# Kernel optimization log

Measured on AMD Instinct MI355X. Metric: run time of the kernel, lower is better.

The kernel has to match this reference:

```python
import jax, jax.numpy as jnp
import numpy as np

B, N, F_IN, D, K, INTER = 64, 512, 128, 128, 32, 256
EPS = 1e-5


def _bn(x, g, b, axes):
    # BatchNorm in training mode (biased batch statistics), matching torch BN forward
    m = x.mean(axis=axes, keepdims=True)
    v = x.var(axis=axes, keepdims=True)
    return (x - m) * jax.lax.rsqrt(v + EPS) * g + b


def setup_inputs() -> dict:
    key = jax.random.key(0)
    ks = jax.random.split(key, 12)
    u = lambda k, s: jax.random.uniform(k, s, jnp.float32, -0.3, 0.3)
    return {
        "data": jax.random.normal(ks[0], (B, N, F_IN), jnp.float32),
        "emb_weight": u(ks[1], (N, D)),          # nn.Embedding(node_num, dim), kaiming-uniform-ish
        "lin_W": u(ks[2], (F_IN, D)),            # GraphLayer lin (no bias)
        "att_i": u(ks[3], (D,)),
        "att_j": u(ks[4], (D,)),
        "att_em_i": u(ks[5], (D,)),
        "att_em_j": u(ks[6], (D,)),
        "gnn_bias": jnp.zeros((D,), jnp.float32),
        "gnn_bn_g": jnp.ones((D,), jnp.float32),
        "gnn_bn_b": jnp.zeros((D,), jnp.float32),
        "bn_out_g": jnp.ones((D,), jnp.float32),
        "bn_out_b": jnp.zeros((D,), jnp.float32),
        "W1": u(ks[7], (D, INTER)), "b1": jnp.zeros((INTER,), jnp.float32),
        "bn1_g": jnp.ones((INTER,), jnp.float32), "bn1_b": jnp.zeros((INTER,), jnp.float32),
        "W2": u(ks[8], (INTER, INTER)), "b2": jnp.zeros((INTER,), jnp.float32),
        "bn2_g": jnp.ones((INTER,), jnp.float32), "bn2_b": jnp.zeros((INTER,), jnp.float32),
        "W3": u(ks[9], (INTER, 1)), "b3": jnp.zeros((1,), jnp.float32),
    }


def reference(data, emb_weight, lin_W, att_i, att_j, att_em_i, att_em_j,
              gnn_bias, gnn_bn_g, gnn_bn_b, bn_out_g, bn_out_b,
              W1, b1, bn1_g, bn1_b, W2, b2, bn2_g, bn2_b, W3, b3):
    M = B * N
    x = data.reshape(M, F_IN)

    # --- learned graph: cosine similarity + topk over DETACHED embeddings ---
    w = jax.lax.stop_gradient(emb_weight)
    nrm = jnp.linalg.norm(w, axis=-1)
    cos = (w @ w.T) / (nrm[:, None] * nrm[None, :])
    topk_idx = jax.lax.top_k(cos, K)[1]                    # [N, K]

    # gated_edge_index = (j=topk neighbor as source, i as target), tiled per batch
    src0 = topk_idx.reshape(-1)                            # [N*K] sources (j)
    dst0 = jnp.repeat(jnp.arange(N), K)                    # [N*K] targets (i)
    off = (jnp.arange(B) * N)[:, None]
    src = (src0[None, :] + off).reshape(-1)                # [B*N*K]
    dst = (dst0[None, :] + off).reshape(-1)
    valid = src != dst                                     # remove_self_loops
    loops = jnp.arange(M)                                  # add_self_loops
    src = jnp.concatenate([src, loops])
    dst = jnp.concatenate([dst, loops])
    valid = jnp.concatenate([valid, jnp.ones((M,), bool)])

    # --- GraphLayer (GAT-style, heads=1, concat=False) ---
    x_lin = x @ lin_W                                      # [M, D]
    emb_b = jnp.tile(emb_weight, (B, 1))                   # [M, D] embedding repeated per batch
    # per-node score halves; gather scalars at edges instead of [E, 2D] keys
    s_i = x_lin @ att_i + emb_b @ att_em_i                 # key_i . cat(att_i, att_em_i)
    s_j = x_lin @ att_j + emb_b @ att_em_j
    logit = jax.nn.leaky_relu(s_i[dst] + s_j[src], 0.2)    # [E]
    logit = jnp.where(valid, logit, -1e9)                  # removed self-edges contribute 0
    mx = jax.ops.segment_max(logit, dst, num_segments=M)
    e = jnp.where(valid, jnp.exp(logit - mx[dst]), 0.0)
    den = jax.ops.segment_sum(e, dst, num_segments=M)
    alpha = e / den[dst]                                   # softmax over incoming edges
    agg = jax.ops.segment_sum(x_lin[src] * alpha[:, None], dst, num_segments=M)
    gcn = jax.nn.relu(_bn(agg + gnn_bias, gnn_bn_g, gnn_bn_b, (0,)))  # GNNLayer bn+relu

    # --- gating by embedding, BN over channel dim, OutLayer MLP ---
    h = gcn.reshape(B, N, D) * emb_weight[None]            # [B, N, D]
    h = jax.nn.relu(_bn(h, bn_out_g, bn_out_b, (0, 1)))    # BatchNorm1d over D channels
    # dropout p=0.2 is identity in eval mode
    o = jax.nn.relu(_bn(h @ W1 + b1, bn1_g, bn1_b, (0, 1)))
    o = jax.nn.relu(_bn(o @ W2 + b2, bn2_g, bn2_b, (0, 1)))
    o = (o @ W3 + b3).reshape(B, N)                        # out.view(-1, node_num)
    return o
```

## Files before the change

kernel.cpp:

```cpp
#include <hip/hip_runtime.h>
#include <math.h>

#define M_ROWS 32768
#define NNODES 512
#define KNBR   32
#define EPSBN  1e-5f

typedef __bf16 bf16x8 __attribute__((ext_vector_type(8)));
typedef __bf16 bf16x4 __attribute__((ext_vector_type(4)));
typedef __bf16 bf16x2 __attribute__((ext_vector_type(2)));
typedef float  f32x4  __attribute__((ext_vector_type(4)));

#if defined(__has_builtin)
#if __has_builtin(__builtin_amdgcn_global_load_lds)
#define HAVE_GLL 1
#endif
#endif

__device__ __forceinline__ void async_ld16(void* lds, const void* g){
#ifdef HAVE_GLL
    __builtin_amdgcn_global_load_lds((__attribute__((address_space(1))) void*)(g),
                                     (__attribute__((address_space(3))) void*)(lds),
                                     16, 0, 0);
#else
    *(bf16x8*)lds = *(const bf16x8*)g;
#endif
}

__global__ void zero_stats_kernel(float* __restrict__ p){
    int t = threadIdx.x;
    for (int i = t; i < 1536; i += 256) p[i] = 0.f;
}

__global__ __launch_bounds__(256) void packw_kernel(const float* __restrict__ lin_W,
                                                    const float* __restrict__ W1,
                                                    const float* __restrict__ W2,
                                                    __bf16* __restrict__ Wp0,
                                                    __bf16* __restrict__ Wp1,
                                                    __bf16* __restrict__ Wp2){
    int gidx = blockIdx.x*256 + threadIdx.x;
    const float* W; __bf16* o; int C, lg;
    if (gidx < 2048)      { W = lin_W; o = Wp0; C = 128; lg = gidx; }
    else if (gidx < 6144) { W = W1;    o = Wp1; C = 256; lg = gidx - 2048; }
    else                  { W = W2;    o = Wp2; C = 256; lg = gidx - 6144; }
    int kg = (C == 128) ? (lg >> 7) : (lg >> 8);
    int c  = lg & (C - 1);
    bf16x8 pk;
    #pragma unroll
    for (int j = 0; j < 8; ++j) pk[j] = (__bf16)W[(size_t)(kg*8 + j)*C + c];
    *(bf16x8*)&o[(size_t)lg*8] = pk;
}

__global__ __launch_bounds__(256) void topk_kernel(const float* __restrict__ emb,
                                                   int* __restrict__ topk){
    __shared__ float wi[128];
    __shared__ float cosv[512];
    int i = blockIdx.x, tid = threadIdx.x;
    if (tid < 128) wi[tid] = emb[i*128 + tid];
    __syncthreads();
    float ni = 0.f;
    #pragma unroll 8
    for (int d = 0; d < 128; ++d) ni += wi[d]*wi[d];
    float rni = sqrtf(ni);
    for (int jj = tid; jj < 512; jj += 256){
        const float4* wj4 = (const float4*)(emb + jj*128);
        float dot = 0.f, nj = 0.f;
        #pragma unroll 8
        for (int d4 = 0; d4 < 32; ++d4){
            float4 w = wj4[d4];
            dot += wi[4*d4+0]*w.x + wi[4*d4+1]*w.y + wi[4*d4+2]*w.z + wi[4*d4+3]*w.w;
            nj  += w.x*w.x + w.y*w.y + w.z*w.z + w.w*w.w;
        }
        cosv[jj] = dot / (rni * sqrtf(nj));
    }
    __syncthreads();
    if (tid < 64){
        int lane = tid;
        float v[8];
        #pragma unroll
        for (int jj = 0; jj < 8; ++jj) v[jj] = cosv[lane + 64*jj];
        for (int k = 0; k < KNBR; ++k){
            float bv = v[0]; int bj = 0;
            #pragma unroll
            for (int jj = 1; jj < 8; ++jj) if (v[jj] > bv){ bv = v[jj]; bj = jj; }
            int bi = lane + 64*bj;
            #pragma unroll
            for (int mask = 1; mask < 64; mask <<= 1){
                float ov = __shfl_xor(bv, mask);
                int   oi = __shfl_xor(bi, mask);
                if (ov > bv || (ov == bv && oi < bi)){ bv = ov; bi = oi; }
            }
            if (lane == 0) topk[i*KNBR + k] = bi;
            if ((bi & 63) == lane){
                int jj = bi >> 6;
                #pragma unroll
                for (int j2 = 0; j2 < 8; ++j2) if (j2 == jj) v[j2] = -2e30f;
            }
        }
    }
}

__global__ __launch_bounds__(128) void embscore_kernel(const float* __restrict__ emb,
                                                       const float* __restrict__ aei,
                                                       const float* __restrict__ aej,
                                                       float* __restrict__ e_i,
                                                       float* __restrict__ e_j){
    __shared__ float si[128], sj[128];
    int n = blockIdx.x, d = threadIdx.x;
    float w = emb[n*128 + d];
    si[d] = w * aei[d];
    sj[d] = w * aej[d];
    __syncthreads();
    for (int s = 64; s > 0; s >>= 1){
        if (d < s){ si[d] += si[d+s]; sj[d] += sj[d+s]; }
        __syncthreads();
    }
    if (d == 0){ e_i[n] = si[0]; e_j[n] = sj[0]; }
}

template<bool ABF16, bool NORM, bool HAS_BIAS, bool STATS, int RT>
__global__ __launch_bounds__(256) void gemm_kernel(
    const void* __restrict__ Av, int a_stride, int Ktot,
    const float* __restrict__ instats,
    const float* __restrict__ gamma, const float* __restrict__ beta,
    const __bf16* __restrict__ Wp, int Ctot,
    const float* __restrict__ bias,
    __bf16* __restrict__ outp,
    float* __restrict__ outstats, int outK)
{
    constexpr int ROWS = RT*64;
    __shared__ __align__(16) __bf16 As[ROWS][136];
    __shared__ __align__(16) __bf16 Bp[16][128][8];
    __shared__ float nsc[128], nsh[128];
    __shared__ float statS[128], statQ[128];

    int tid  = threadIdx.x;
    int lane = tid & 63, wv = tid >> 6;
    int mrow = lane & 15, q = lane >> 4;
    int cb0  = blockIdx.y * 128;
    int row0 = blockIdx.x * ROWS;

    f32x4 acc[RT][8];
    #pragma unroll
    for (int rt = 0; rt < RT; ++rt)
        #pragma unroll
        for (int ct = 0; ct < 8; ++ct)
            acc[rt][ct] = (f32x4){0.f,0.f,0.f,0.f};

    for (int kc = 0; kc < Ktot; kc += 128){
        if (NORM && tid < 128){
            int f = kc + tid;
            float mean = instats[f] * (1.f/32768.f);
            float var  = instats[Ktot + f] * (1.f/32768.f) - mean*mean;
            float sc   = gamma[f] / sqrtf(var + EPSBN);
            nsc[tid] = sc;
            nsh[tid] = beta[f] - mean*sc;
        }
        __syncthreads();

        int kg0 = kc >> 3;
        #pragma unroll
        for (int i = 0; i < 8; ++i){
            int p = tid + i*256;
            const __bf16* src = Wp + ((size_t)(kg0 + (p>>7))*Ctot + cb0 + (p&127))*8;
            async_ld16((__bf16*)Bp + (size_t)p*8, src);
        }
        if (ABF16){
            const __bf16* A = (const __bf16*)Av;
            #pragma unroll
            for (int i = 0; i < ROWS/16; ++i){
                int p = tid + i*256;
                int r = p >> 4, c8 = p & 15;
                bf16x8 v = *(const bf16x8*)&A[(size_t)(row0 + r)*a_stride + kc + c8*8];
                if (NORM){
                    bf16x8 o;
                    #pragma unroll
                    for (int j = 0; j < 8; ++j){
                        int f = c8*8 + j;
                        o[j] = (__bf16)fmaxf((float)v[j]*nsc[f] + nsh[f], 0.f);
                    }
                    v = o;
                }
                *(bf16x8*)&As[r][c8*8] = v;
            }
        } else {
            const float* A = (const float*)Av;
            #pragma unroll
            for (int i = 0; i < ROWS/16; ++i){
                int p = tid + i*256;
                int r = p >> 4, c8 = p & 15;
                const float* src = &A[(size_t)(row0 + r)*a_stride + kc + c8*8];
                float4 a0 = *(const float4*)src;
                float4 a1 = *(const float4*)(src + 4);
                bf16x8 o;
                o[0]=(__bf16)a0.x; o[1]=(__bf16)a0.y; o[2]=(__bf16)a0.z; o[3]=(__bf16)a0.w;
                o[4]=(__bf16)a1.x; o[5]=(__bf16)a1.y; o[6]=(__bf16)a1.z; o[7]=(__bf16)a1.w;
                *(bf16x8*)&As[r][c8*8] = o;
            }
        }
        __syncthreads();

        #pragma unroll
        for (int ks = 0; ks < 4; ++ks){
            bf16x8 a[RT];
            #pragma unroll
            for (int rt = 0; rt < RT; ++rt)
                a[rt] = *(const bf16x8*)&As[wv*(RT*16) + rt*16 + mrow][ks*32 + q*8];
            #pragma unroll
            for (int ct = 0; ct < 8; ++ct){
                bf16x8 bb = *(const bf16x8*)&Bp[ks*4 + q][ct*16 + mrow][0];
                #pragma unroll
                for (int rt = 0; rt < RT; ++rt)
                    acc[rt][ct] = __builtin_amdgcn_mfma_f32_16x16x32_bf16(a[rt], bb, acc[rt][ct], 0, 0, 0);
            }
        }
    }

    if (STATS){
        if (tid < 128){ statS[tid] = 0.f; statQ[tid] = 0.f; }
        __syncthreads();
    }

    float cs[8] = {0,0,0,0,0,0,0,0}, cq[8] = {0,0,0,0,0,0,0,0};
    #pragma unroll
    for (int ct = 0; ct < 8; ++ct){
        int col = cb0 + ct*16 + mrow;
        float bv = HAS_BIAS ? bias[col] : 0.f;
        #pragma unroll
        for (int rt = 0; rt < RT; ++rt){
            #pragma unroll
            for (int reg = 0; reg < 4; ++reg){
                int row = row0 + wv*(RT*16) + rt*16 + q*4 + reg;
                __bf16 bvv = (__bf16)(acc[rt][ct][reg] + bv);
                outp[(size_t)row*Ctot + col] = bvv;
                if (STATS){ float fv = (float)bvv; cs[ct] += fv; cq[ct] += fv*fv; }
            }
        }
    }
    if (STATS){
        #pragma unroll
        for (int ct = 0; ct < 8; ++ct){
            float s  = cs[ct]; s  += __shfl_xor(s, 16);  s  += __shfl_xor(s, 32);
            float qq = cq[ct]; qq += __shfl_xor(qq, 16); qq += __shfl_xor(qq, 32);
            if (q == 0){
                atomicAdd(&statS[ct*16 + mrow], s);
                atomicAdd(&statQ[ct*16 + mrow], qq);
            }
        }
        __syncthreads();
        if (tid < 128){
            atomicAdd(&outstats[cb0 + tid],        statS[tid]);
            atomicAdd(&outstats[outK + cb0 + tid], statQ[tid]);
        }
    }
}

__global__ __launch_bounds__(256) void score_kernel(const __bf16* __restrict__ xl,
                                                    const float2* __restrict__ att_i2,
                                                    const float2* __restrict__ att_j2,
                                                    const float* __restrict__ e_i,
                                                    const float* __restrict__ e_j,
                                                    float* __restrict__ s_i,
                                                    float* __restrict__ s_j){
    int gid = blockIdx.x*256 + threadIdx.x;
    int wid = gid >> 6, lane = gid & 63;
    bf16x2 v = *(const bf16x2*)&xl[(size_t)wid*128 + lane*2];
    float2 ai2 = att_i2[lane], aj2 = att_j2[lane];
    float vx = (float)v[0], vy = (float)v[1];
    float ai = vx*ai2.x + vy*ai2.y;
    float aj = vx*aj2.x + vy*aj2.y;
    for (int off = 32; off; off >>= 1){
        ai += __shfl_down(ai, off);
        aj += __shfl_down(aj, off);
    }
    if (lane == 0){
        int n = wid & 511;
        s_i[wid] = ai + e_i[n];
        s_j[wid] = aj + e_j[n];
    }
}

__global__ __launch_bounds__(256) void agg_kernel(const __bf16* __restrict__ xl,
                                                  const float* __restrict__ s_i,
                                                  const float* __restrict__ s_j,
                                                  const int* __restrict__ topk,
                                                  const float2* __restrict__ gnn_bias2,
                                                  __bf16* __restrict__ aggp){
    int gid  = blockIdx.x*256 + threadIdx.x;
    int m    = gid >> 6, lane = gid & 63;
    int b = m >> 9, i = m & 511;
    int src; bool valid;
    if (lane < KNBR){ int j = topk[i*KNBR + lane]; src = (b << 9) + j; valid = (j != i); }
    else            { src = m; valid = (lane == KNBR); }
    float l = s_i[m] + s_j[src];
    l = (l >= 0.f) ? l : 0.2f*l;
    l = valid ? l : -1e30f;
    float mx = l;
    #pragma unroll
    for (int mask = 1; mask < 64; mask <<= 1) mx = fmaxf(mx, __shfl_xor(mx, mask));
    float e = valid ? __expf(l - mx) : 0.f;
    float den = e;
    #pragma unroll
    for (int mask = 1; mask < 64; mask <<= 1) den += __shfl_xor(den, mask);
    float alpha = e / den;

    float2 acc = make_float2(0.f, 0.f);
    #pragma unroll 4
    for (int k = 0; k < 33; ++k){
        float a = __shfl(alpha, k);
        int   s = __shfl(src, k);
        bf16x2 v = *(const bf16x2*)&xl[(size_t)s*128 + lane*2];
        acc.x += a*(float)v[0]; acc.y += a*(float)v[1];
    }
    float2 bv = gnn_bias2[lane];
    bf16x2 o;
    o[0] = (__bf16)(acc.x + bv.x);
    o[1] = (__bf16)(acc.y + bv.y);
    *(bf16x2*)&aggp[(size_t)m*128 + lane*2] = o;
}

__global__ __launch_bounds__(256) void colstats_kernel(const __bf16* __restrict__ X,
                                                       float* __restrict__ st){
    int tid = threadIdx.x;
    int cg = tid & 31, rs = tid >> 5;
    int c0 = cg*4;
    float s[4] = {0,0,0,0}, qq[4] = {0,0,0,0};
    for (int m = blockIdx.x*8 + rs; m < M_ROWS; m += gridDim.x*8){
        bf16x4 v = *(const bf16x4*)&X[(size_t)m*128 + c0];
        #pragma unroll
        for (int j = 0; j < 4; ++j){ float f = (float)v[j]; s[j] += f; qq[j] += f*f; }
    }
    __shared__ float rS[8][128], rQ[8][128];
    #pragma unroll
    for (int j = 0; j < 4; ++j){ rS[rs][c0+j] = s[j]; rQ[rs][c0+j] = qq[j]; }
    __syncthreads();
    if (tid < 128){
        float ts = 0.f, tq = 0.f;
        #pragma unroll
        for (int u = 0; u < 8; ++u){ ts += rS[u][tid]; tq += rQ[u][tid]; }
        atomicAdd(&st[tid],       ts);
        atomicAdd(&st[128 + tid], tq);
    }
}

__global__ __launch_bounds__(256) void gate_kernel(const __bf16* __restrict__ agg,
                                                   const float* __restrict__ gst,
                                                   const float* __restrict__ g,
                                                   const float* __restrict__ bta,
                                                   const float* __restrict__ emb,
                                                   __bf16* __restrict__ h,
                                                   float* __restrict__ hstats){
    int tid = threadIdx.x;
    int cg = tid & 31, rs = tid >> 5;
    int c0 = cg*4;
    float sc[4], sh[4];
    #pragma unroll
    for (int j = 0; j < 4; ++j){
        float mean = gst[c0+j] * (1.f/32768.f);
        float var  = gst[128 + c0+j] * (1.f/32768.f) - mean*mean;
        sc[j] = g[c0+j] / sqrtf(var + EPSBN);
        sh[j] = bta[c0+j] - mean*sc[j];
    }
    float s[4] = {0,0,0,0}, qq[4] = {0,0,0,0};
    for (int m = blockIdx.x*8 + rs; m < M_ROWS; m += gridDim.x*8){
        bf16x4 v = *(const bf16x4*)&agg[(size_t)m*128 + c0];
        float4 e = *(const float4*)&emb[(size_t)(m & 511)*128 + c0];
        float f0 = fmaxf((float)v[0]*sc[0] + sh[0], 0.f) * e.x;
        float f1 = fmaxf((float)v[1]*sc[1] + sh[1], 0.f) * e.y;
        float f2 = fmaxf((float)v[2]*sc[2] + sh[2], 0.f) * e.z;
        float f3 = fmaxf((float)v[3]*sc[3] + sh[3], 0.f) * e.w;
        bf16x4 o; o[0]=(__bf16)f0; o[1]=(__bf16)f1; o[2]=(__bf16)f2; o[3]=(__bf16)f3;
        *(bf16x4*)&h[(size_t)m*128 + c0] = o;
        float r0=(float)o[0], r1=(float)o[1], r2=(float)o[2], r3=(float)o[3];
        s[0]+=r0; qq[0]+=r0*r0; s[1]+=r1; qq[1]+=r1*r1;
        s[2]+=r2; qq[2]+=r2*r2; s[3]+=r3; qq[3]+=r3*r3;
    }
    __shared__ float rS[8][128], rQ[8][128];
    #pragma unroll
    for (int j = 0; j < 4; ++j){ rS[rs][c0+j] = s[j]; rQ[rs][c0+j] = qq[j]; }
    __syncthreads();
    if (tid < 128){
        float ts = 0.f, tq = 0.f;
        #pragma unroll
        for (int u = 0; u < 8; ++u){ ts += rS[u][tid]; tq += rQ[u][tid]; }
        atomicAdd(&hstats[tid],       ts);
        atomicAdd(&hstats[128 + tid], tq);
    }
}

__global__ __launch_bounds__(256) void final_kernel(const __bf16* __restrict__ t2,
                                                    const float* __restrict__ st,
                                                    const float* __restrict__ g,
                                                    const float* __restrict__ bta,
                                                    const float* __restrict__ W3,
                                                    const float* __restrict__ b3,
                                                    float* __restrict__ outp){
    int gid = blockIdx.x*256 + threadIdx.x;
    int wid = gid >> 6, lane = gid & 63;
    int c0 = lane*4;
    bf16x4 v  = *(const bf16x4*)&t2[(size_t)wid*256 + c0];
    float4 w3 = *(const float4*)&W3[c0];
    float4 gg = *(const float4*)&g[c0];
    float4 bb = *(const float4*)&bta[c0];
    float4 sm = *(const float4*)&st[c0];
    float4 sq = *(const float4*)&st[256 + c0];
    float accv = 0.f;
    {
        float mean, var, val;
        mean = sm.x*(1.f/32768.f); var = sq.x*(1.f/32768.f) - mean*mean;
        val = ((float)v[0]-mean)*(gg.x/sqrtf(var+EPSBN)) + bb.x; accv += fmaxf(val,0.f)*w3.x;
        mean = sm.y*(1.f/32768.f); var = sq.y*(1.f/32768.f) - mean*mean;
        val = ((float)v[1]-mean)*(gg.y/sqrtf(var+EPSBN)) + bb.y; accv += fmaxf(val,0.f)*w3.y;
        mean = sm.z*(1.f/32768.f); var = sq.z*(1.f/32768.f) - mean*mean;
        val = ((float)v[2]-mean)*(gg.z/sqrtf(var+EPSBN)) + bb.z; accv += fmaxf(val,0.f)*w3.z;
        mean = sm.w*(1.f/32768.f); var = sq.w*(1.f/32768.f) - mean*mean;
        val = ((float)v[3]-mean)*(gg.w/sqrtf(var+EPSBN)) + bb.w; accv += fmaxf(val,0.f)*w3.w;
    }
    for (int off = 32; off; off >>= 1) accv += __shfl_down(accv, off);
    if (lane == 0) outp[wid] = accv + b3[0];
}

extern "C" void kernel_launch(void* const* d_in, const int* in_sizes, int n_in,
                              void* d_out, int out_size, void* d_ws, size_t ws_size,
                              hipStream_t stream)
{
    (void)in_sizes; (void)n_in; (void)out_size; (void)ws_size;
    const float* data   = (const float*)d_in[0];
    const float* emb    = (const float*)d_in[1];
    const float* lin_W  = (const float*)d_in[2];
    const float* att_i  = (const float*)d_in[3];
    const float* att_j  = (const float*)d_in[4];
    const float* aem_i  = (const float*)d_in[5];
    const float* aem_j  = (const float*)d_in[6];
    const float* gnn_bias = (const float*)d_in[7];
    const float* gnn_g  = (const float*)d_in[8];
    const float* gnn_b  = (const float*)d_in[9];
    const float* bno_g  = (const float*)d_in[10];
    const float* bno_b  = (const float*)d_in[11];
    const float* W1     = (const float*)d_in[12];
    const float* b1     = (const float*)d_in[13];
    const float* bn1_g  = (const float*)d_in[14];
    const float* bn1_b  = (const float*)d_in[15];
    const float* W2     = (const float*)d_in[16];
    const float* b2     = (const float*)d_in[17];
    const float* bn2_g  = (const float*)d_in[18];
    const float* bn2_b  = (const float*)d_in[19];
    const float* W3     = (const float*)d_in[20];
    const float* b3     = (const float*)d_in[21];
    float* outp = (float*)d_out;
    char*  ws   = (char*)d_ws;

    int*    topk     = (int*)ws;
    float*  e_i      = (float*)(ws + 65536);
    float*  e_j      = (float*)(ws + 67584);
    float*  s_i      = (float*)(ws + 69632);
    float*  s_j      = (float*)(ws + 200704);
    float*  stats    = (float*)(ws + 331776);
    float*  gnnstats = stats;
    float*  hstats   = stats + 256;
    float*  bn1stats = stats + 512;
    float*  bn2stats = stats + 1024;
    __bf16* Wp0      = (__bf16*)(ws + 337920);
    __bf16* Wp1      = (__bf16*)(ws + 370688);
    __bf16* Wp2      = (__bf16*)(ws + 436224);
    __bf16* xlin     = (__bf16*)(ws + 1048576);
    __bf16* aggb     = (__bf16*)(ws + 1048576 +   8388608);
    __bf16* h        = (__bf16*)(ws + 1048576 + 2*8388608);
    __bf16* t1       = (__bf16*)(ws + 1048576 + 3*8388608);
    __bf16* t2       = (__bf16*)(ws + 1048576 + 3*8388608 + 16777216);

    zero_stats_kernel<<<1, 256, 0, stream>>>(stats);
    packw_kernel<<<56, 256, 0, stream>>>(lin_W, W1, W2, Wp0, Wp1, Wp2);
    topk_kernel<<<NNODES, 256, 0, stream>>>(emb, topk);
    embscore_kernel<<<NNODES, 128, 0, stream>>>(emb, aem_i, aem_j, e_i, e_j);

    gemm_kernel<false,false,false,false,1><<<dim3(512,1), 256, 0, stream>>>(
        data, 128, 128, nullptr, nullptr, nullptr, Wp0, 128, nullptr, xlin, nullptr, 0);

    score_kernel<<<M_ROWS/4, 256, 0, stream>>>(xlin, (const float2*)att_i,
                                               (const float2*)att_j, e_i, e_j, s_i, s_j);
    agg_kernel<<<M_ROWS/4, 256, 0, stream>>>(xlin, s_i, s_j, topk,
                                             (const float2*)gnn_bias, aggb);
    colstats_kernel<<<256, 256, 0, stream>>>(aggb, gnnstats);
    gate_kernel<<<256, 256, 0, stream>>>(aggb, gnnstats, gnn_g, gnn_b, emb, h, hstats);

    gemm_kernel<true,true,true,true,2><<<dim3(256,2), 256, 0, stream>>>(
        h, 128, 128, hstats, bno_g, bno_b, Wp1, 256, b1, t1, bn1stats, 256);

    gemm_kernel<true,true,true,true,2><<<dim3(256,2), 256, 0, stream>>>(
        t1, 256, 256, bn1stats, bn1_g, bn1_b, Wp2, 256, b2, t2, bn2stats, 256);

    final_kernel<<<M_ROWS/4, 256, 0, stream>>>(t2, bn2stats, bn2_g, bn2_b, W3, b3, outp);
}
```

Before: 265.0 us.

## Fuse setup kernels, score into xlin GEMM, and gating into first MLP GEMM

Merges zero-stats, weight packing, topk and embedding-score kernels into one setup launch. Computes attention scores in the xlin GEMM epilogue from fp32 accumulators, and stops materialising the gated h tensor: hstats only gathers statistics, and the first MLP GEMM recomputes BN+ReLU+gate+BN+ReLU while loading A. This removes several launches and an 8MB write/read of h, at the cost of extra per-element arithmetic and emb loads in the GEMM A-load path. Stats now use unrounded fp32 values, which slightly changes numerics.

Result: faster. 259.6 us (-2.0%).

```diff
diff --git a/kernel.cpp b/kernel.cpp
--- a/kernel.cpp
+++ b/kernel.cpp
@@ -27,35 +27,38 @@
 #endif
 }
 
-__global__ void zero_stats_kernel(float* __restrict__ p){
-    int t = threadIdx.x;
-    for (int i = t; i < 1536; i += 256) p[i] = 0.f;
-}
-
-__global__ __launch_bounds__(256) void packw_kernel(const float* __restrict__ lin_W,
-                                                    const float* __restrict__ W1,
-                                                    const float* __restrict__ W2,
-                                                    __bf16* __restrict__ Wp0,
-                                                    __bf16* __restrict__ Wp1,
-                                                    __bf16* __restrict__ Wp2){
-    int gidx = blockIdx.x*256 + threadIdx.x;
-    const float* W; __bf16* o; int C, lg;
-    if (gidx < 2048)      { W = lin_W; o = Wp0; C = 128; lg = gidx; }
-    else if (gidx < 6144) { W = W1;    o = Wp1; C = 256; lg = gidx - 2048; }
-    else                  { W = W2;    o = Wp2; C = 256; lg = gidx - 6144; }
-    int kg = (C == 128) ? (lg >> 7) : (lg >> 8);
-    int c  = lg & (C - 1);
-    bf16x8 pk;
-    #pragma unroll
-    for (int j = 0; j < 8; ++j) pk[j] = (__bf16)W[(size_t)(kg*8 + j)*C + c];
-    *(bf16x8*)&o[(size_t)lg*8] = pk;
-}
-
-__global__ __launch_bounds__(256) void topk_kernel(const float* __restrict__ emb,
-                                                   int* __restrict__ topk){
+__global__ __launch_bounds__(256) void setup_kernel(
+    const float* __restrict__ emb,
+    const float* __restrict__ aei, const float* __restrict__ aej,
+    const float* __restrict__ lin_W, const float* __restrict__ W1,
+    const float* __restrict__ W2,
+    int* __restrict__ topk, float* __restrict__ e_i, float* __restrict__ e_j,
+    __bf16* __restrict__ Wp0, __bf16* __restrict__ Wp1, __bf16* __restrict__ Wp2,
+    float* __restrict__ stats)
+{
+    int bid = blockIdx.x, tid = threadIdx.x;
+    if (bid >= 512){
+        if (bid == 568){
+            for (int i = tid; i < 1536; i += 256) stats[i] = 0.f;
+            return;
+        }
+        int gidx = (bid - 512)*256 + tid;
+        const float* W; __bf16* o; int C, lg;
+        if (gidx < 2048)      { W = lin_W; o = Wp0; C = 128; lg = gidx; }
+        else if (gidx < 6144) { W = W1;    o = Wp1; C = 256; lg = gidx - 2048; }
+        else                  { W = W2;    o = Wp2; C = 256; lg = gidx - 6144; }
+        int kg = (C == 128) ? (lg >> 7) : (lg >> 8);
+        int c  = lg & (C - 1);
+        bf16x8 pk;
+        #pragma unroll
+        for (int j = 0; j < 8; ++j) pk[j] = (__bf16)W[(size_t)(kg*8 + j)*C + c];
+        *(bf16x8*)&o[(size_t)lg*8] = pk;
+        return;
+    }
+
     __shared__ float wi[128];
     __shared__ float cosv[512];
-    int i = blockIdx.x, tid = threadIdx.x;
+    int i = bid;
     if (tid < 128) wi[tid] = emb[i*128 + tid];
     __syncthreads();
     float ni = 0.f;
@@ -97,64 +100,144 @@
                 for (int j2 = 0; j2 < 8; ++j2) if (j2 == jj) v[j2] = -2e30f;
             }
         }
-    }
-}
-
-__global__ __launch_bounds__(128) void embscore_kernel(const float* __restrict__ emb,
-                                                       const float* __restrict__ aei,
-                                                       const float* __restrict__ aej,
-                                                       float* __restrict__ e_i,
-                                                       float* __restrict__ e_j){
-    __shared__ float si[128], sj[128];
-    int n = blockIdx.x, d = threadIdx.x;
-    float w = emb[n*128 + d];
-    si[d] = w * aei[d];
-    sj[d] = w * aej[d];
-    __syncthreads();
-    for (int s = 64; s > 0; s >>= 1){
-        if (d < s){ si[d] += si[d+s]; sj[d] += sj[d+s]; }
-        __syncthreads();
-    }
-    if (d == 0){ e_i[n] = si[0]; e_j[n] = sj[0]; }
-}
-
-template<bool ABF16, bool NORM, bool HAS_BIAS, bool STATS, int RT>
-__global__ __launch_bounds__(256) void gemm_kernel(
-    const void* __restrict__ Av, int a_stride, int Ktot,
-    const float* __restrict__ instats,
-    const float* __restrict__ gamma, const float* __restrict__ beta,
+    } else if (tid < 128){
+        int lane = tid - 64;
+        float ai = wi[lane]*aei[lane] + wi[lane+64]*aei[lane+64];
+        float aj = wi[lane]*aej[lane] + wi[lane+64]*aej[lane+64];
+        for (int off = 32; off; off >>= 1){
+            ai += __shfl_down(ai, off);
+            aj += __shfl_down(aj, off);
+        }
+        if (lane == 0){ e_i[i] = ai; e_j[i] = aj; }
+    }
+}
+
+__global__ __launch_bounds__(256) void xlin_gemm_kernel(
+    const float* __restrict__ A,
+    const __bf16* __restrict__ Wp,
+    const float* __restrict__ att_i, const float* __restrict__ att_j,
+    const float* __restrict__ e_i,   const float* __restrict__ e_j,
+    __bf16* __restrict__ outp,
+    float* __restrict__ s_i, float* __restrict__ s_j)
+{
+    __shared__ __align__(16) __bf16 As[64][136];
+    __shared__ __align__(16) __bf16 Bp[16][128][8];
+
+    int tid  = threadIdx.x;
+    int lane = tid & 63, wv = tid >> 6;
+    int mrow = lane & 15, q = lane >> 4;
+    int row0 = blockIdx.x * 64;
+
+    f32x4 acc[8];
+    #pragma unroll
+    for (int ct = 0; ct < 8; ++ct) acc[ct] = (f32x4){0.f,0.f,0.f,0.f};
+
+    #pragma unroll
+    for (int i = 0; i < 8; ++i){
+        int p = tid + i*256;
+        const __bf16* src = Wp + ((size_t)(p>>7)*128 + (p&127))*8;
+        async_ld16((__bf16*)Bp + (size_t)p*8, src);
+    }
+    #pragma unroll
+    for (int i = 0; i < 4; ++i){
+        int p = tid + i*256;
+        int r = p >> 4, c8 = p & 15;
+        const float* src = &A[(size_t)(row0 + r)*128 + c8*8];
+        float4 a0 = *(const float4*)src;
+        float4 a1 = *(const float4*)(src + 4);
+        bf16x8 o;
+        o[0]=(__bf16)a0.x; o[1]=(__bf16)a0.y; o[2]=(__bf16)a0.z; o[3]=(__bf16)a0.w;
+        o[4]=(__bf16)a1.x; o[5]=(__bf16)a1.y; o[6]=(__bf16)a1.z; o[7]=(__bf16)a1.w;
+        *(bf16x8*)&As[r][c8*8] = o;
+    }
+    __syncthreads();
+
+    #pragma unroll
+    for (int ks = 0; ks < 4; ++ks){
+        bf16x8 a = *(const bf16x8*)&As[wv*16 + mrow][ks*32 + q*8];
+        #pragma unroll
+        for (int ct = 0; ct < 8; ++ct){
+            bf16x8 bb = *(const bf16x8*)&Bp[ks*4 + q][ct*16 + mrow][0];
+            acc[ct] = __builtin_amdgcn_mfma_f32_16x16x32_bf16(a, bb, acc[ct], 0, 0, 0);
+        }
+    }
+
+    float ai[4] = {0,0,0,0}, aj[4] = {0,0,0,0};
+    #pragma unroll
+    for (int ct = 0; ct < 8; ++ct){
+        int col = ct*16 + mrow;
+        float wti = att_i[col], wtj = att_j[col];
+        #pragma unroll
+        for (int reg = 0; reg < 4; ++reg){
+            int row = row0 + wv*16 + q*4 + reg;
+            float v = acc[ct][reg];
+            outp[(size_t)row*128 + col] = (__bf16)v;
+            ai[reg] += v*wti; aj[reg] += v*wtj;
+        }
+    }
+    #pragma unroll
+    for (int mask = 1; mask < 16; mask <<= 1){
+        #pragma unroll
+        for (int reg = 0; reg < 4; ++reg){
+            ai[reg] += __shfl_xor(ai[reg], mask);
+            aj[reg] += __shfl_xor(aj[reg], mask);
+        }
+    }
+    if (mrow == 0){
+        #pragma unroll
+        for (int reg = 0; reg < 4; ++reg){
+            int row = row0 + wv*16 + q*4 + reg;
+            int n = row & 511;
+            s_i[row] = ai[reg] + e_i[n];
+            s_j[row] = aj[reg] + e_j[n];
+        }
+    }
+}
+
+template<bool GATE>
+__global__ __launch_bounds__(256) void gemm2_kernel(
+    const __bf16* __restrict__ A, int a_stride, int Ktot,
+    const float* __restrict__ st1, const float* __restrict__ g1, const float* __restrict__ b1,
+    const float* __restrict__ emb,
+    const float* __restrict__ st2, const float* __restrict__ g2, const float* __restrict__ b2,
     const __bf16* __restrict__ Wp, int Ctot,
     const float* __restrict__ bias,
     __bf16* __restrict__ outp,
     float* __restrict__ outstats, int outK)
 {
-    constexpr int ROWS = RT*64;
-    __shared__ __align__(16) __bf16 As[ROWS][136];
+    __shared__ __align__(16) __bf16 As[128][136];
     __shared__ __align__(16) __bf16 Bp[16][128][8];
-    __shared__ float nsc[128], nsh[128];
+    __shared__ float nsc1[128], nsh1[128], nsc2[128], nsh2[128];
     __shared__ float statS[128], statQ[128];
 
     int tid  = threadIdx.x;
     int lane = tid & 63, wv = tid >> 6;
     int mrow = lane & 15, q = lane >> 4;
     int cb0  = blockIdx.y * 128;
-    int row0 = blockIdx.x * ROWS;
-
-    f32x4 acc[RT][8];
-    #pragma unroll
-    for (int rt = 0; rt < RT; ++rt)
+    int row0 = blockIdx.x * 128;
+
+    f32x4 acc[2][8];
+    #pragma unroll
+    for (int rt = 0; rt < 2; ++rt)
         #pragma unroll
         for (int ct = 0; ct < 8; ++ct)
             acc[rt][ct] = (f32x4){0.f,0.f,0.f,0.f};
 
     for (int kc = 0; kc < Ktot; kc += 128){
-        if (NORM && tid < 128){
+        if (tid < 128){
             int f = kc + tid;
-            float mean = instats[f] * (1.f/32768.f);
-            float var  = instats[Ktot + f] * (1.f/32768.f) - mean*mean;
-            float sc   = gamma[f] / sqrtf(var + EPSBN);
-            nsc[tid] = sc;
-            nsh[tid] = beta[f] - mean*sc;
+            float mean = st1[f] * (1.f/32768.f);
+            float var  = st1[Ktot + f] * (1.f/32768.f) - mean*mean;
+            float sc   = g1[f] / sqrtf(var + EPSBN);
+            nsc1[tid] = sc;
+            nsh1[tid] = b1[f] - mean*sc;
+            if (GATE){
+                float mean2 = st2[tid] * (1.f/32768.f);
+                float var2  = st2[128 + tid] * (1.f/32768.f) - mean2*mean2;
+                float sc2   = g2[tid] / sqrtf(var2 + EPSBN);
+                nsc2[tid] = sc2;
+                nsh2[tid] = b2[tid] - mean2*sc2;
+            }
         }
         __syncthreads();
 
@@ -165,118 +248,80 @@
             const __bf16* src = Wp + ((size_t)(kg0 + (p>>7))*Ctot + cb0 + (p&127))*8;
             async_ld16((__bf16*)Bp + (size_t)p*8, src);
         }
-        if (ABF16){
-            const __bf16* A = (const __bf16*)Av;
-            #pragma unroll
-            for (int i = 0; i < ROWS/16; ++i){
-                int p = tid + i*256;
-                int r = p >> 4, c8 = p & 15;
-                bf16x8 v = *(const bf16x8*)&A[(size_t)(row0 + r)*a_stride + kc + c8*8];
-                if (NORM){
-                    bf16x8 o;
-                    #pragma unroll
-                    for (int j = 0; j < 8; ++j){
-                        int f = c8*8 + j;
-                        o[j] = (__bf16)fmaxf((float)v[j]*nsc[f] + nsh[f], 0.f);
-                    }
-                    v = o;
+        #pragma unroll
+        for (int i = 0; i < 8; ++i){
+            int p = tid + i*256;
+            int r = p >> 4, c8 = p & 15;
+            bf16x8 v = *(const bf16x8*)&A[(size_t)(row0 + r)*a_stride + kc + c8*8];
+            bf16x8 o;
+            if (GATE){
+                const float* ep = &emb[(size_t)((row0 + r) & 511)*128 + c8*8];
+                float4 e0 = *(const float4*)ep;
+                float4 e1 = *(const float4*)(ep + 4);
+                float ee[8] = {e0.x,e0.y,e0.z,e0.w,e1.x,e1.y,e1.z,e1.w};
+                #pragma unroll
+                for (int j = 0; j < 8; ++j){
+                    int f = c8*8 + j;
+                    float hv = fmaxf((float)v[j]*nsc1[f] + nsh1[f], 0.f) * ee[j];
+                    o[j] = (__bf16)fmaxf(hv*nsc2[f] + nsh2[f], 0.f);
                 }
-                *(bf16x8*)&As[r][c8*8] = v;
+            } else {
+                #pragma unroll
+                for (int j = 0; j < 8; ++j){
+                    int f = c8*8 + j;
+                    o[j] = (__bf16)fmaxf((float)v[j]*nsc1[f] + nsh1[f], 0.f);
+                }
             }
-        } else {
-            const float* A = (const float*)Av;
-            #pragma unroll
-            for (int i = 0; i < ROWS/16; ++i){
-                int p = tid + i*256;
-                int r = p >> 4, c8 = p & 15;
-                const float* src = &A[(size_t)(row0 + r)*a_stride + kc + c8*8];
-                float4 a0 = *(const float4*)src;
-                float4 a1 = *(const float4*)(src + 4);
-                bf16x8 o;
-                o[0]=(__bf16)a0.x; o[1]=(__bf16)a0.y; o[2]=(__bf16)a0.z; o[3]=(__bf16)a0.w;
-                o[4]=(__bf16)a1.x; o[5]=(__bf16)a1.y; o[6]=(__bf16)a1.z; o[7]=(__bf16)a1.w;
-                *(bf16x8*)&As[r][c8*8] = o;
-            }
+            *(bf16x8*)&As[r][c8*8] = o;
         }
         __syncthreads();
 
         #pragma unroll
         for (int ks = 0; ks < 4; ++ks){
-            bf16x8 a[RT];
-            #pragma unroll
-            for (int rt = 0; rt < RT; ++rt)
-                a[rt] = *(const bf16x8*)&As[wv*(RT*16) + rt*16 + mrow][ks*32 + q*8];
+            bf16x8 a0 = *(const bf16x8*)&As[wv*32      + mrow][ks*32 + q*8];
+            bf16x8 a1 = *(const bf16x8*)&As[wv*32 + 16 + mrow][ks*32 + q*8];
             #pragma unroll
             for (int ct = 0; ct < 8; ++ct){
                 bf16x8 bb = *(const bf16x8*)&Bp[ks*4 + q][ct*16 + mrow][0];
-                #pragma unroll
-                for (int rt = 0; rt < RT; ++rt)
-                    acc[rt][ct] = __builtin_amdgcn_mfma_f32_16x16x32_bf16(a[rt], bb, acc[rt][ct], 0, 0, 0);
+                acc[0][ct] = __builtin_amdgcn_mfma_f32_16x16x32_bf16(a0, bb, acc[0][ct], 0, 0, 0);
+                acc[1][ct] = __builtin_amdgcn_mfma_f32_16x16x32_bf16(a1, bb, acc[1][ct], 0, 0, 0);
             }
         }
-    }
-
-    if (STATS){
-        if (tid < 128){ statS[tid] = 0.f; statQ[tid] = 0.f; }
         __syncthreads();
     }
+
+    if (tid < 128){ statS[tid] = 0.f; statQ[tid] = 0.f; }
+    __syncthreads();
 
     float cs[8] = {0,0,0,0,0,0,0,0}, cq[8] = {0,0,0,0,0,0,0,0};
     #pragma unroll
     for (int ct = 0; ct < 8; ++ct){
         int col = cb0 + ct*16 + mrow;
-        float bv = HAS_BIAS ? bias[col] : 0.f;
-        #pragma unroll
-        for (int rt = 0; rt < RT; ++rt){
+        float bv = bias[col];
+        #pragma unroll
+        for (int rt = 0; rt < 2; ++rt){
             #pragma unroll
             for (int reg = 0; reg < 4; ++reg){
-                int row = row0 + wv*(RT*16) + rt*16 + q*4 + reg;
+                int row = row0 + wv*32 + rt*16 + q*4 + reg;
                 __bf16 bvv = (__bf16)(acc[rt][ct][reg] + bv);
                 outp[(size_t)row*Ctot + col] = bvv;
-                if (STATS){ float fv = (float)bvv; cs[ct] += fv; cq[ct] += fv*fv; }
+                float fv = (float)bvv; cs[ct] += fv; cq[ct] += fv*fv;
             }
         }
     }
-    if (STATS){
-        #pragma unroll
-        for (int ct = 0; ct < 8; ++ct){
-            float s  = cs[ct]; s  += __shfl_xor(s, 16);  s  += __shfl_xor(s, 32);
-            float qq = cq[ct]; qq += __shfl_xor(qq, 16); qq += __shfl_xor(qq, 32);
-            if (q == 0){
-                atomicAdd(&statS[ct*16 + mrow], s);
-                atomicAdd(&statQ[ct*16 + mrow], qq);
-            }
-        }
-        __syncthreads();
-        if (tid < 128){
-            atomicAdd(&outstats[cb0 + tid],        statS[tid]);
-            atomicAdd(&outstats[outK + cb0 + tid], statQ[tid]);
-        }
-    }
-}
-
-__global__ __launch_bounds__(256) void score_kernel(const __bf16* __restrict__ xl,
-                                                    const float2* __restrict__ att_i2,
-                                                    const float2* __restrict__ att_j2,
-                                                    const float* __restrict__ e_i,
-                                                    const float* __restrict__ e_j,
-                                                    float* __restrict__ s_i,
-                                                    float* __restrict__ s_j){
-    int gid = blockIdx.x*256 + threadIdx.x;
-    int wid = gid >> 6, lane = gid & 63;
-    bf16x2 v = *(const bf16x2*)&xl[(size_t)wid*128 + lane*2];
-    float2 ai2 = att_i2[lane], aj2 = att_j2[lane];
-    float vx = (float)v[0], vy = (float)v[1];
-    float ai = vx*ai2.x + vy*ai2.y;
-    float aj = vx*aj2.x + vy*aj2.y;
-    for (int off = 32; off; off >>= 1){
-        ai += __shfl_down(ai, off);
-        aj += __shfl_down(aj, off);
-    }
-    if (lane == 0){
-        int n = wid & 511;
-        s_i[wid] = ai + e_i[n];
-        s_j[wid] = aj + e_j[n];
+    #pragma unroll
+    for (int ct = 0; ct < 8; ++ct){
+        float s  = cs[ct]; s  += __shfl_xor(s, 16);  s  += __shfl_xor(s, 32);
+        float qq = cq[ct]; qq += __shfl_xor(qq, 16); qq += __shfl_xor(qq, 32);
+        if (q == 0){
+            atomicAdd(&statS[ct*16 + mrow], s);
+            atomicAdd(&statQ[ct*16 + mrow], qq);
+        }
+    }
+    __syncthreads();
+    if (tid < 128){
+        atomicAdd(&outstats[cb0 + tid],        statS[tid]);
+        atomicAdd(&outstats[outK + cb0 + tid], statQ[tid]);
     }
 }
 
@@ -343,13 +388,12 @@
     }
 }
 
-__global__ __launch_bounds__(256) void gate_kernel(const __bf16* __restrict__ agg,
-                                                   const float* __restrict__ gst,
-                                                   const float* __restrict__ g,
-                                                   const float* __restrict__ bta,
-                                                   const float* __restrict__ emb,
-                                                   __bf16* __restrict__ h,
-                                                   float* __restrict__ hstats){
+__global__ __launch_bounds__(256) void hstats_kernel(const __bf16* __restrict__ agg,
+                                                     const float* __restrict__ gst,
+                                                     const float* __restrict__ g,
+                                                     const float* __restrict__ bta,
+                                                     const float* __restrict__ emb,
+                                                     float* __restrict__ hstats){
     int tid = threadIdx.x;
     int cg = tid & 31, rs = tid >> 5;
     int c0 = cg*4;
@@ -369,11 +413,8 @@
         float f1 = fmaxf((float)v[1]*sc[1] + sh[1], 0.f) * e.y;
         float f2 = fmaxf((float)v[2]*sc[2] + sh[2], 0.f) * e.z;
         float f3 = fmaxf((float)v[3]*sc[3] + sh[3], 0.f) * e.w;
-        bf16x4 o; o[0]=(__bf16)f0; o[1]=(__bf16)f1; o[2]=(__bf16)f2; o[3]=(__bf16)f3;
-        *(bf16x4*)&h[(size_t)m*128 + c0] = o;
-        float r0=(float)o[0], r1=(float)o[1], r2=(float)o[2], r3=(float)o[3];
-        s[0]+=r0; qq[0]+=r0*r0; s[1]+=r1; qq[1]+=r1*r1;
-        s[2]+=r2; qq[2]+=r2*r2; s[3]+=r3; qq[3]+=r3*r3;
+        s[0]+=f0; qq[0]+=f0*f0; s[1]+=f1; qq[1]+=f1*f1;
+        s[2]+=f2; qq[2]+=f2*f2; s[3]+=f3; qq[3]+=f3*f3;
     }
     __shared__ float rS[8][128], rQ[8][128];
     #pragma unroll
@@ -465,30 +506,27 @@
     __bf16* Wp2      = (__bf16*)(ws + 436224);
     __bf16* xlin     = (__bf16*)(ws + 1048576);
     __bf16* aggb     = (__bf16*)(ws + 1048576 +   8388608);
-    __bf16* h        = (__bf16*)(ws + 1048576 + 2*8388608);
-    __bf16* t1       = (__bf16*)(ws + 1048576 + 3*8388608);
-    __bf16* t2       = (__bf16*)(ws + 1048576 + 3*8388608 + 16777216);
-
-    zero_stats_kernel<<<1, 256, 0, stream>>>(stats);
-    packw_kernel<<<56, 256, 0, stream>>>(lin_W, W1, W2, Wp0, Wp1, Wp2);
-    topk_kernel<<<NNODES, 256, 0, stream>>>(emb, topk);
-    embscore_kernel<<<NNODES, 128, 0, stream>>>(emb, aem_i, aem_j, e_i, e_j);
-
-    gemm_kernel<false,false,false,false,1><<<dim3(512,1), 256, 0, stream>>>(
-        data, 128, 128, nullptr, nullptr, nullptr, Wp0, 128, nullptr, xlin, nullptr, 0);
-
-    score_kernel<<<M_ROWS/4, 256, 0, stream>>>(xlin, (const float2*)att_i,
-                                               (const float2*)att_j, e_i, e_j, s_i, s_j);
+    __bf16* t1       = (__bf16*)(ws + 1048576 + 2*8388608);
+    __bf16* t2       = (__bf16*)(ws + 1048576 + 2*8388608 + 16777216);
+
+    setup_kernel<<<569, 256, 0, stream>>>(emb, aem_i, aem_j, lin_W, W1, W2,
+                                          topk, e_i, e_j, Wp0, Wp1, Wp2, stats);
+
+    xlin_gemm_kernel<<<512, 256, 0, stream>>>(data, Wp0, att_i, att_j, e_i, e_j,
+                                              xlin, s_i, s_j);
+
     agg_kernel<<<M_ROWS/4, 256, 0, stream>>>(xlin, s_i, s_j, topk,
                                              (const float2*)gnn_bias, aggb);
     colstats_kernel<<<256, 256, 0, stream>>>(aggb, gnnstats);
-    gate_kernel<<<256, 256, 0, stream>>>(aggb, gnnstats, gnn_g, gnn_b, emb, h, hstats);
-
-    gemm_kernel<true,true,true,true,2><<<dim3(256,2), 256, 0, stream>>>(
-        h, 128, 128, hstats, bno_g, bno_b, Wp1, 256, b1, t1, bn1stats, 256);
-
-    gemm_kernel<true,true,true,true,2><<<dim3(256,2), 256, 0, stream>>>(
-        t1, 256, 256, bn1stats, bn1_g, bn1_b, Wp2, 256, b2, t2, bn2stats, 256);
+    hstats_kernel<<<256, 256, 0, stream>>>(aggb, gnnstats, gnn_g, gnn_b, emb, hstats);
+
+    gemm2_kernel<true><<<dim3(256,2), 256, 0, stream>>>(
+        aggb, 128, 128, gnnstats, gnn_g, gnn_b, emb, hstats, bno_g, bno_b,
+        Wp1, 256, b1, t1, bn1stats, 256);
+
+    gemm2_kernel<false><<<dim3(256,2), 256, 0, stream>>>(
+        t1, 256, 256, bn1stats, bn1_g, bn1_b, nullptr, nullptr, nullptr, nullptr,
+        Wp2, 256, b2, t2, bn2stats, 256);
 
     final_kernel<<<M_ROWS/4, 256, 0, stream>>>(t2, bn2stats, bn2_g, bn2_b, W3, b3, outp);
 }
```
